# Kernel tuning notes

Measured on AMD Instinct MI355X. Metric: run time of the kernel, lower is better.

## Reference

```python
import jax, jax.numpy as jnp
import numpy as np

B, Q, K, H, V = 16, 128, 512, 256, 256


def setup_inputs() -> dict:
    key = jax.random.key(0)
    ks = jax.random.split(key, 7)
    return {
        "queries": jax.random.normal(ks[0], (B, Q, H), dtype=jnp.float32),
        "keys": jax.random.normal(ks[1], (B, K, H), dtype=jnp.float32),
        "values": jax.random.normal(ks[2], (B, K, V), dtype=jnp.float32),
        "Wq": jax.random.normal(ks[3], (H, H), dtype=jnp.float32) / np.sqrt(H),
        "Wk": jax.random.normal(ks[4], (H, H), dtype=jnp.float32) / np.sqrt(H),
        "Wv": jax.random.normal(ks[5], (H,), dtype=jnp.float32) / np.sqrt(H),
        "valid_lens": jax.random.randint(ks[6], (B,), 1, K + 1, dtype=jnp.int32),
    }


def reference(queries, keys, values, Wq, Wk, Wv, valid_lens):
    # Projections (no bias, matching nn.Linear(..., bias=False))
    q = jnp.einsum("bqd,hd->bqh", queries, Wq)  # W_q: weight is [out,in] in torch; symmetric here
    k = jnp.einsum("bkd,hd->bkh", keys, Wk)
    # Broadcast add -> tanh -> project to scalar score: [B, Q, K]
    features = jnp.tanh(q[:, :, None, :] + k[:, None, :, :])  # [B,Q,K,H]
    scores = jnp.einsum("bqkh,h->bqk", features, Wv)
    # masked_softmax: positions >= valid_len get -1e6 before softmax
    mask = jnp.arange(K)[None, None, :] < valid_lens[:, None, None]  # [B,1,K]
    scores = jnp.where(mask, scores, -1e6)
    attn = jax.nn.softmax(scores, axis=-1)
    # dropout in eval mode = identity
    return jnp.einsum("bqk,bkv->bqv", attn, values)
```

## Files before the change

kernel.cpp:

```cpp
#include <hip/hip_runtime.h>

#define BQ   16
#define QLEN 128
#define KLEN 512
#define HD   256
#define VD   256

typedef __bf16 bf16x8 __attribute__((ext_vector_type(8)));
typedef __bf16 bf16x4 __attribute__((ext_vector_type(4)));
typedef float  f32x4  __attribute__((ext_vector_type(4)));

static __device__ __forceinline__ float fexp2(float x) {
#if __has_builtin(__builtin_amdgcn_exp2f)
    return __builtin_amdgcn_exp2f(x);
#else
    return exp2f(x);
#endif
}
static __device__ __forceinline__ float frcp(float x) {
#if __has_builtin(__builtin_amdgcn_rcpf)
    return __builtin_amdgcn_rcpf(x);
#else
    return 1.0f / x;
#endif
}

#define EXP_SCALE 2.8853900817779268f

__global__ __launch_bounds__(256) void conv_w(
    const float* __restrict__ Wq, const float* __restrict__ Wk,
    __bf16* __restrict__ hi, __bf16* __restrict__ lo)
{
    const int t = blockIdx.x * 256 + threadIdx.x;
    const int e = t * 4;
    const float* src = (e < 65536) ? (Wq + e) : (Wk + (e - 65536));
    float4 v = *(const float4*)src;
    float f[4] = {v.x, v.y, v.z, v.w};
    bf16x4 h, l;
    #pragma unroll
    for (int j = 0; j < 4; ++j) {
        __bf16 hv = (__bf16)f[j];
        h[j] = hv;
        l[j] = (__bf16)(f[j] - (float)hv);
    }
    *(bf16x4*)(hi + e) = h;
    *(bf16x4*)(lo + e) = l;
}

__global__ __launch_bounds__(256) void mfma_proj(
    const float* __restrict__ queries, const float* __restrict__ keys,
    const __bf16* __restrict__ Whi_g, const __bf16* __restrict__ Wlo_g,
    float* __restrict__ Eq, float* __restrict__ Ekt)
{
    __shared__ __bf16 Ahi_s[64][40];
    __shared__ __bf16 Alo_s[64][40];
    __shared__ __bf16 Whi_s[128][40];
    __shared__ __bf16 Wlo_s[128][40];

    const int t    = threadIdx.x;
    const int ln   = t & 63;
    const int w    = t >> 6;
    const int p    = ln & 15;
    const int quad = ln >> 4;
    const int bx = blockIdx.x, by = blockIdx.y;
    const bool isq = by < 32;
    const int row0 = by * 64;
    const int col0 = bx * 128;

    const float* Ag = isq ? (queries + (size_t)row0 * HD)
                          : (keys + (size_t)(row0 - 2048) * HD);
    const __bf16* Wh = Whi_g + (isq ? 0 : 65536);
    const __bf16* Wl = Wlo_g + (isq ? 0 : 65536);

    const int ar = t >> 2, ac = (t & 3) * 8;
    const int wr = t >> 1, wc = (t & 1) * 16;

    float4 pa0, pa1;
    uint4 ph0, ph1, pl0, pl1;
    {
        const float* ap = Ag + ar * HD + ac;
        pa0 = *(const float4*)ap;
        pa1 = *(const float4*)(ap + 4);
        const size_t wb = (size_t)(col0 + wr) * HD + wc;
        ph0 = *(const uint4*)(Wh + wb);
        ph1 = *(const uint4*)(Wh + wb + 8);
        pl0 = *(const uint4*)(Wl + wb);
        pl1 = *(const uint4*)(Wl + wb + 8);
    }

    f32x4 acc[4][2] = {};

    for (int s = 0; s < 8; ++s) {
        __syncthreads();
        {
            float f[8] = {pa0.x, pa0.y, pa0.z, pa0.w, pa1.x, pa1.y, pa1.z, pa1.w};
            bf16x8 h, l;
            #pragma unroll
            for (int j = 0; j < 8; ++j) {
                __bf16 hv = (__bf16)f[j];
                h[j] = hv;
                l[j] = (__bf16)(f[j] - (float)hv);
            }
            *(bf16x8*)&Ahi_s[ar][ac] = h;
            *(bf16x8*)&Alo_s[ar][ac] = l;
            *(uint4*)&Whi_s[wr][wc]     = ph0;
            *(uint4*)&Whi_s[wr][wc + 8] = ph1;
            *(uint4*)&Wlo_s[wr][wc]     = pl0;
            *(uint4*)&Wlo_s[wr][wc + 8] = pl1;
        }
        __syncthreads();
        if (s < 7) {
            const int kc = (s + 1) * 32;
            const float* ap = Ag + ar * HD + kc + ac;
            pa0 = *(const float4*)ap;
            pa1 = *(const float4*)(ap + 4);
            const size_t wb = (size_t)(col0 + wr) * HD + kc + wc;
            ph0 = *(const uint4*)(Wh + wb);
            ph1 = *(const uint4*)(Wh + wb + 8);
            pl0 = *(const uint4*)(Wl + wb);
            pl1 = *(const uint4*)(Wl + wb + 8);
        }
        bf16x8 ah[4], al[4], bh[2], bl[2];
        #pragma unroll
        for (int mi = 0; mi < 4; ++mi) {
            ah[mi] = *(const bf16x8*)&Ahi_s[mi * 16 + p][quad * 8];
            al[mi] = *(const bf16x8*)&Alo_s[mi * 16 + p][quad * 8];
        }
        #pragma unroll
        for (int ci = 0; ci < 2; ++ci) {
            const int hrow = w * 32 + ci * 16 + p;
            bh[ci] = *(const bf16x8*)&Whi_s[hrow][quad * 8];
            bl[ci] = *(const bf16x8*)&Wlo_s[hrow][quad * 8];
        }
        #pragma unroll
        for (int mi = 0; mi < 4; ++mi)
            #pragma unroll
            for (int ci = 0; ci < 2; ++ci) {
                acc[mi][ci] = __builtin_amdgcn_mfma_f32_16x16x32_bf16(ah[mi], bh[ci], acc[mi][ci], 0, 0, 0);
                acc[mi][ci] = __builtin_amdgcn_mfma_f32_16x16x32_bf16(ah[mi], bl[ci], acc[mi][ci], 0, 0, 0);
                acc[mi][ci] = __builtin_amdgcn_mfma_f32_16x16x32_bf16(al[mi], bh[ci], acc[mi][ci], 0, 0, 0);
            }
    }

    #pragma unroll
    for (int mi = 0; mi < 4; ++mi)
        #pragma unroll
        for (int ci = 0; ci < 2; ++ci) {
            const int H  = col0 + w * 32 + ci * 16 + p;
            const int rl = mi * 16 + quad * 4;
            float e0 = fexp2(acc[mi][ci][0] * EXP_SCALE);
            float e1 = fexp2(acc[mi][ci][1] * EXP_SCALE);
            float e2 = fexp2(acc[mi][ci][2] * EXP_SCALE);
            float e3 = fexp2(acc[mi][ci][3] * EXP_SCALE);
            if (isq) {
                float* dst = Eq + (size_t)(row0 + rl) * HD + H;
                dst[0] = e0; dst[HD] = e1; dst[2 * HD] = e2; dst[3 * HD] = e3;
            } else {
                const int kr = row0 - 2048 + rl;
                const int b = kr >> 9, k0 = kr & 511;
                float4 st; st.x = e0; st.y = e1; st.z = e2; st.w = e3;
                *(float4*)(Ekt + ((size_t)b * HD + H) * KLEN + k0) = st;
            }
        }
}

__global__ __launch_bounds__(256) void proj_exp_gemm(
    const float* __restrict__ Qin, const float* __restrict__ Kin,
    const float* __restrict__ Wq, const float* __restrict__ Wk,
    float* __restrict__ Eq, float* __restrict__ Ekt)
{
    __shared__ union {
        struct { float a[2][16][68]; float w[2][16][68]; } s;
        float tb[64][65];
    } sh;

    const int t  = threadIdx.x;
    const int tx = t & 15, ty = t >> 4;
    const int bx = blockIdx.x, by = blockIdx.y;
    const bool isq = by < 32;
    const int row0 = isq ? by * 64 : (by - 32) * 64;
    const float* A = isq ? Qin : Kin;
    const float* W = isq ? Wq : Wk;
    const int lrow = t >> 2, ld0 = (t & 3) * 4;
    const float* Ab = A + (row0 + lrow) * HD;
    const float* Wb = W + (bx * 64 + lrow) * HD;

    float4 av = *(const float4*)(Ab + ld0);
    float4 wv = *(const float4*)(Wb + ld0);
    sh.s.a[0][ld0 + 0][lrow] = av.x; sh.s.a[0][ld0 + 1][lrow] = av.y;
    sh.s.a[0][ld0 + 2][lrow] = av.z; sh.s.a[0][ld0 + 3][lrow] = av.w;
    sh.s.w[0][ld0 + 0][lrow] = wv.x; sh.s.w[0][ld0 + 1][lrow] = wv.y;
    sh.s.w[0][ld0 + 2][lrow] = wv.z; sh.s.w[0][ld0 + 3][lrow] = wv.w;

    float acc[4][4] = {};
    int p = 0;
    for (int kc = 0; kc < HD; kc += 16) {
        if (kc + 16 < HD) {
            av = *(const float4*)(Ab + kc + 16 + ld0);
            wv = *(const float4*)(Wb + kc + 16 + ld0);
        }
        __syncthreads();
        if (kc + 16 < HD) {
            const int np = p ^ 1;
            sh.s.a[np][ld0 + 0][lrow] = av.x; sh.s.a[np][ld0 + 1][lrow] = av.y;
            sh.s.a[np][ld0 + 2][lrow] = av.z; sh.s.a[np][ld0 + 3][lrow] = av.w;
            sh.s.w[np][ld0 + 0][lrow] = wv.x; sh.s.w[np][ld0 + 1][lrow] = wv.y;
            sh.s.w[np][ld0 + 2][lrow] = wv.z; sh.s.w[np][ld0 + 3][lrow] = wv.w;
        }
        #pragma unroll
        for (int dd = 0; dd < 16; ++dd) {
            float4 a4 = *(const float4*)&sh.s.a[p][dd][ty * 4];
            float4 w4 = *(const float4*)&sh.s.w[p][dd][tx * 4];
            const float* af = (const float*)&a4;
            const float* wf = (const float*)&w4;
            #pragma unroll
            for (int i = 0; i < 4; ++i)
                #pragma unroll
                for (int j = 0; j < 4; ++j)
                    acc[i][j] = fmaf(af[i], wf[j], acc[i][j]);
        }
        p ^= 1;
    }

    float e[4][4];
    #pragma unroll
    for (int i = 0; i < 4; ++i)
        #pragma unroll
        for (int j = 0; j < 4; ++j)
            e[i][j] = fexp2(acc[i][j] * EXP_SCALE);

    if (isq) {
        float* Cb = Eq + (row0 + ty * 4) * HD + bx * 64 + tx * 4;
        #pragma unroll
        for (int i = 0; i < 4; ++i) {
            float4 st; st.x = e[i][0]; st.y = e[i][1]; st.z = e[i][2]; st.w = e[i][3];
            *(float4*)(Cb + i * HD) = st;
        }
    } else {
        __syncthreads();
        #pragma unroll
        for (int j = 0; j < 4; ++j) {
            float4 st; st.x = e[0][j]; st.y = e[1][j]; st.z = e[2][j]; st.w = e[3][j];
            *(float4*)&sh.tb[tx * 4 + j][ty * 4] = st;
        }
        __syncthreads();
        const int r = t >> 2, c0 = (t & 3) * 16;
        const int b = row0 >> 9, kbase = row0 & 511;
        float* dst = Ekt + ((size_t)b * HD + bx * 64 + r) * KLEN + kbase + c0;
        #pragma unroll
        for (int u = 0; u < 4; ++u) {
            float4 v = *(const float4*)&sh.tb[r][c0 + u * 4];
            *(float4*)(dst + u * 4) = v;
        }
    }
}

__global__ __launch_bounds__(512, 4) void fused_attn(
    const float* __restrict__ Eq, const float* __restrict__ Ekt,
    const float* __restrict__ values, const float* __restrict__ Wv,
    const int* __restrict__ vlen, float* __restrict__ out)
{
    __shared__ float eq_s[4][HD];
    __shared__ float wv_s[HD];
    __shared__ float sc[4][KLEN];
    __shared__ float ps[4][4][KLEN];
    __shared__ float wred[4];

    const int t    = threadIdx.x;
    const int b    = blockIdx.x >> 5;
    const int q0   = (blockIdx.x & 31) * 4;
    const int lane = t & 63;
    const int wid  = t >> 6;

    {
        const int h = t & 255, rr = t >> 8;
        eq_s[rr][h]     = Eq[(b * QLEN + q0 + rr) * HD + h];
        eq_s[rr + 2][h] = Eq[(b * QLEN + q0 + rr + 2) * HD + h];
        if (t < HD) {
            float w = Wv[t];
            wv_s[t] = w;
            float ws = w;
            #pragma unroll
            for (int off = 32; off > 0; off >>= 1) ws += __shfl_xor(ws, off, 64);
            if (lane == 0) wred[wid] = ws;
        }
    }
    __syncthreads();
    const float wv_sum = wred[0] + wred[1] + wred[2] + wred[3];

    const int hs    = wid & 3, khalf = wid >> 2;
    const int hbase = hs * 64;
    const int k4    = khalf * 256 + lane * 4;
    const float* ek = Ekt + ((size_t)b * HD + hbase) * KLEN + k4;
    float acc[4][4] = {};
    for (int hh = 0; hh < 64; hh += 4) {
        float4 e0 = *(const float4*)(ek + (size_t)(hh + 0) * KLEN);
        float4 e1 = *(const float4*)(ek + (size_t)(hh + 1) * KLEN);
        float4 e2 = *(const float4*)(ek + (size_t)(hh + 2) * KLEN);
        float4 e3 = *(const float4*)(ek + (size_t)(hh + 3) * KLEN);
        const float* E0 = (const float*)&e0;
        const float* E1 = (const float*)&e1;
        const float* E2 = (const float*)&e2;
        const float* E3 = (const float*)&e3;
        const float w0 = wv_s[hbase + hh + 0], w1 = wv_s[hbase + hh + 1];
        const float w2 = wv_s[hbase + hh + 2], w3 = wv_s[hbase + hh + 3];
        #pragma unroll
        for (int i = 0; i < 4; ++i) {
            const float a0 = eq_s[i][hbase + hh + 0], a1 = eq_s[i][hbase + hh + 1];
            const float a2 = eq_s[i][hbase + hh + 2], a3 = eq_s[i][hbase + hh + 3];
            #pragma unroll
            for (int j = 0; j < 4; ++j) {
                float d0 = fmaf(a0, E0[j], 1.f);
                float d1 = fmaf(a1, E1[j], 1.f);
                float d2 = fmaf(a2, E2[j], 1.f);
                float d3 = fmaf(a3, E3[j], 1.f);
                float d01 = d0 * d1, d23 = d2 * d3;
                float n01 = fmaf(w1, d0, w0 * d1);
                float n23 = fmaf(w3, d2, w2 * d3);
                float top = fmaf(n23, d01, n01 * d23);
                acc[i][j] = fmaf(top, frcp(d01 * d23), acc[i][j]);
            }
        }
    }
    #pragma unroll
    for (int i = 0; i < 4; ++i) {
        float4 st; st.x = acc[i][0]; st.y = acc[i][1]; st.z = acc[i][2]; st.w = acc[i][3];
        *(float4*)&ps[hs][i][k4] = st;
    }
    __syncthreads();

    {
        const int q = t >> 7, kk = (t & 127) * 4;
        float4 s0 = *(const float4*)&ps[0][q][kk];
        float4 s1 = *(const float4*)&ps[1][q][kk];
        float4 s2 = *(const float4*)&ps[2][q][kk];
        float4 s3 = *(const float4*)&ps[3][q][kk];
        float4 r;
        r.x = fmaf(-2.f, s0.x + s1.x + s2.x + s3.x, wv_sum);
        r.y = fmaf(-2.f, s0.y + s1.y + s2.y + s3.y, wv_sum);
        r.z = fmaf(-2.f, s0.z + s1.z + s2.z + s3.z, wv_sum);
        r.w = fmaf(-2.f, s0.w + s1.w + s2.w + s3.w, wv_sum);
        *(float4*)&sc[q][kk] = r;
    }
    __syncthreads();

    if (wid < 4) {
        const int len = vlen[b];
        float s[8];
        float m = -3.0e38f;
        #pragma unroll
        for (int j = 0; j < 8; ++j) {
            int k = lane + j * 64;
            float v = sc[wid][k];
            v = (k < len) ? v : -1.0e6f;
            s[j] = v;
            m = fmaxf(m, v);
        }
        #pragma unroll
        for (int off = 32; off > 0; off >>= 1) m = fmaxf(m, __shfl_xor(m, off, 64));
        float sum = 0.f;
        #pragma unroll
        for (int j = 0; j < 8; ++j) {
            float ev = fexp2(1.4426950408889634f * (s[j] - m));
            s[j] = ev;
            sum += ev;
        }
        #pragma unroll
        for (int off = 32; off > 0; off >>= 1) sum += __shfl_xor(sum, off, 64);
        const float rs = frcp(sum);
        #pragma unroll
        for (int j = 0; j < 8; ++j) sc[wid][lane + j * 64] = s[j] * rs;
    }
    __syncthreads();

    float (*po)[4][VD] = (float (*)[4][VD])ps;
    const int c4 = lane * 4;
    const float* vb = values + (size_t)b * KLEN * VD + (size_t)(wid * 64) * VD + c4;
    float o[4][4] = {};
    for (int kk = 0; kk < 64; kk += 4) {
        const int k = wid * 64 + kk;
        float4 pr[4];
        pr[0] = *(const float4*)&sc[0][k];
        pr[1] = *(const float4*)&sc[1][k];
        pr[2] = *(const float4*)&sc[2][k];
        pr[3] = *(const float4*)&sc[3][k];
        #pragma unroll
        for (int j = 0; j < 4; ++j) {
            float4 v4 = *(const float4*)(vb + (size_t)(kk + j) * VD);
            #pragma unroll
            for (int r = 0; r < 4; ++r) {
                float pj = ((const float*)&pr[r])[j];
                o[r][0] = fmaf(pj, v4.x, o[r][0]);
                o[r][1] = fmaf(pj, v4.y, o[r][1]);
                o[r][2] = fmaf(pj, v4.z, o[r][2]);
                o[r][3] = fmaf(pj, v4.w, o[r][3]);
            }
        }
    }
    #pragma unroll
    for (int r = 0; r < 4; ++r) {
        float4 st; st.x = o[r][0]; st.y = o[r][1]; st.z = o[r][2]; st.w = o[r][3];
        *(float4*)&po[wid][r][c4] = st;
    }
    __syncthreads();

    #pragma unroll
    for (int u = 0; u < 2; ++u) {
        int idx = t + u * 512;
        int r = idx >> 8, c = idx & 255;
        float s = 0.f;
        #pragma unroll
        for (int sl = 0; sl < 8; ++sl) s += po[sl][r][c];
        out[(b * QLEN + q0 + r) * VD + c] = s;
    }
}

extern "C" void kernel_launch(void* const* d_in, const int* in_sizes, int n_in,
                              void* d_out, int out_size, void* d_ws, size_t ws_size,
                              hipStream_t stream) {
    const float* queries = (const float*)d_in[0];
    const float* keys    = (const float*)d_in[1];
    const float* values  = (const float*)d_in[2];
    const float* Wq      = (const float*)d_in[3];
    const float* Wk      = (const float*)d_in[4];
    const float* Wv      = (const float*)d_in[5];
    const int*   vl      = (const int*)d_in[6];
    float* out = (float*)d_out;

    float* Eq  = (float*)d_ws;
    float* Ekt = Eq + 2048 * 256;

    if (ws_size >= 11010048) {
        __bf16* Whi = (__bf16*)(Ekt + 16 * HD * KLEN);
        __bf16* Wlo = Whi + 131072;
        conv_w<<<dim3(128), 256, 0, stream>>>(Wq, Wk, Whi, Wlo);
        mfma_proj<<<dim3(2, 160), 256, 0, stream>>>(queries, keys, Whi, Wlo, Eq, Ekt);
    } else {
        proj_exp_gemm<<<dim3(4, 160), 256, 0, stream>>>(queries, keys, Wq, Wk, Eq, Ekt);
    }
    fused_attn<<<dim3(512), 512, 0, stream>>>(Eq, Ekt, values, Wv, vl, out);
}
```

Baseline: 123.9 us.

## Fuse weight split into projection and skip masked key work by valid length

Removes the separate weight-conversion kernel and instead splits the fp32 weights into bf16 hi/lo parts inside the projection kernel. Key projection tiles lying wholly beyond the valid length return early, and the attention kernel skips score and value accumulation for key ranges past valid_len, zero-filling partial sums. The block-index mapping is reordered so batches interleave across blocks, which spreads the uneven per-batch work more evenly. Masked keys get a softmax weight of exactly zero, so skipping them is legitimate. The cost is redundant weight conversion in every block and some extra branching.

```diff
diff --git a/kernel.cpp b/kernel.cpp
--- a/kernel.cpp
+++ b/kernel.cpp
@@ -27,29 +27,10 @@
 
 #define EXP_SCALE 2.8853900817779268f
 
-__global__ __launch_bounds__(256) void conv_w(
-    const float* __restrict__ Wq, const float* __restrict__ Wk,
-    __bf16* __restrict__ hi, __bf16* __restrict__ lo)
-{
-    const int t = blockIdx.x * 256 + threadIdx.x;
-    const int e = t * 4;
-    const float* src = (e < 65536) ? (Wq + e) : (Wk + (e - 65536));
-    float4 v = *(const float4*)src;
-    float f[4] = {v.x, v.y, v.z, v.w};
-    bf16x4 h, l;
-    #pragma unroll
-    for (int j = 0; j < 4; ++j) {
-        __bf16 hv = (__bf16)f[j];
-        h[j] = hv;
-        l[j] = (__bf16)(f[j] - (float)hv);
-    }
-    *(bf16x4*)(hi + e) = h;
-    *(bf16x4*)(lo + e) = l;
-}
-
 __global__ __launch_bounds__(256) void mfma_proj(
     const float* __restrict__ queries, const float* __restrict__ keys,
-    const __bf16* __restrict__ Whi_g, const __bf16* __restrict__ Wlo_g,
+    const float* __restrict__ Wq, const float* __restrict__ Wk,
+    const int* __restrict__ vlen,
     float* __restrict__ Eq, float* __restrict__ Ekt)
 {
     __shared__ __bf16 Ahi_s[64][40];
@@ -67,25 +48,26 @@
     const int row0 = by * 64;
     const int col0 = bx * 128;
 
+    if (!isq) {
+        const int kr0 = row0 - 2048;
+        if ((kr0 & 511) >= vlen[kr0 >> 9]) return;
+    }
+
     const float* Ag = isq ? (queries + (size_t)row0 * HD)
                           : (keys + (size_t)(row0 - 2048) * HD);
-    const __bf16* Wh = Whi_g + (isq ? 0 : 65536);
-    const __bf16* Wl = Wlo_g + (isq ? 0 : 65536);
+    const float* Wg = isq ? Wq : Wk;
 
     const int ar = t >> 2, ac = (t & 3) * 8;
     const int wr = t >> 1, wc = (t & 1) * 16;
 
-    float4 pa0, pa1;
-    uint4 ph0, ph1, pl0, pl1;
+    float4 pa0, pa1, pw0, pw1, pw2, pw3;
     {
         const float* ap = Ag + ar * HD + ac;
         pa0 = *(const float4*)ap;
         pa1 = *(const float4*)(ap + 4);
-        const size_t wb = (size_t)(col0 + wr) * HD + wc;
-        ph0 = *(const uint4*)(Wh + wb);
-        ph1 = *(const uint4*)(Wh + wb + 8);
-        pl0 = *(const uint4*)(Wl + wb);
-        pl1 = *(const uint4*)(Wl + wb + 8);
+        const float* wp = Wg + (size_t)(col0 + wr) * HD + wc;
+        pw0 = *(const float4*)wp;       pw1 = *(const float4*)(wp + 4);
+        pw2 = *(const float4*)(wp + 8); pw3 = *(const float4*)(wp + 12);
     }
 
     f32x4 acc[4][2] = {};
@@ -93,20 +75,33 @@
     for (int s = 0; s < 8; ++s) {
         __syncthreads();
         {
-            float f[8] = {pa0.x, pa0.y, pa0.z, pa0.w, pa1.x, pa1.y, pa1.z, pa1.w};
+            float fa[8] = {pa0.x, pa0.y, pa0.z, pa0.w, pa1.x, pa1.y, pa1.z, pa1.w};
             bf16x8 h, l;
             #pragma unroll
             for (int j = 0; j < 8; ++j) {
-                __bf16 hv = (__bf16)f[j];
+                __bf16 hv = (__bf16)fa[j];
                 h[j] = hv;
-                l[j] = (__bf16)(f[j] - (float)hv);
+                l[j] = (__bf16)(fa[j] - (float)hv);
             }
             *(bf16x8*)&Ahi_s[ar][ac] = h;
             *(bf16x8*)&Alo_s[ar][ac] = l;
-            *(uint4*)&Whi_s[wr][wc]     = ph0;
-            *(uint4*)&Whi_s[wr][wc + 8] = ph1;
-            *(uint4*)&Wlo_s[wr][wc]     = pl0;
-            *(uint4*)&Wlo_s[wr][wc + 8] = pl1;
+
+            float fw[16] = {pw0.x, pw0.y, pw0.z, pw0.w, pw1.x, pw1.y, pw1.z, pw1.w,
+                            pw2.x, pw2.y, pw2.z, pw2.w, pw3.x, pw3.y, pw3.z, pw3.w};
+            bf16x8 wh0, wh1, wl0, wl1;
+            #pragma unroll
+            for (int j = 0; j < 8; ++j) {
+                __bf16 hv = (__bf16)fw[j];
+                wh0[j] = hv;
+                wl0[j] = (__bf16)(fw[j] - (float)hv);
+                __bf16 hv1 = (__bf16)fw[8 + j];
+                wh1[j] = hv1;
+                wl1[j] = (__bf16)(fw[8 + j] - (float)hv1);
+            }
+            *(bf16x8*)&Whi_s[wr][wc]     = wh0;
+            *(bf16x8*)&Whi_s[wr][wc + 8] = wh1;
+            *(bf16x8*)&Wlo_s[wr][wc]     = wl0;
+            *(bf16x8*)&Wlo_s[wr][wc + 8] = wl1;
         }
         __syncthreads();
         if (s < 7) {
@@ -114,11 +109,9 @@
             const float* ap = Ag + ar * HD + kc + ac;
             pa0 = *(const float4*)ap;
             pa1 = *(const float4*)(ap + 4);
-            const size_t wb = (size_t)(col0 + wr) * HD + kc + wc;
-            ph0 = *(const uint4*)(Wh + wb);
-            ph1 = *(const uint4*)(Wh + wb + 8);
-            pl0 = *(const uint4*)(Wl + wb);
-            pl1 = *(const uint4*)(Wl + wb + 8);
+            const float* wp = Wg + (size_t)(col0 + wr) * HD + kc + wc;
+            pw0 = *(const float4*)wp;       pw1 = *(const float4*)(wp + 4);
+            pw2 = *(const float4*)(wp + 8); pw3 = *(const float4*)(wp + 12);
         }
         bf16x8 ah[4], al[4], bh[2], bl[2];
         #pragma unroll
@@ -267,10 +260,11 @@
     __shared__ float wred[4];
 
     const int t    = threadIdx.x;
-    const int b    = blockIdx.x >> 5;
-    const int q0   = (blockIdx.x & 31) * 4;
+    const int b    = blockIdx.x & 15;
+    const int q0   = (blockIdx.x >> 4) * 4;
     const int lane = t & 63;
     const int wid  = t >> 6;
+    const int len  = vlen[b];
 
     {
         const int h = t & 255, rr = t >> 8;
@@ -289,43 +283,45 @@
     const float wv_sum = wred[0] + wred[1] + wred[2] + wred[3];
 
     const int hs    = wid & 3, khalf = wid >> 2;
-    const int hbase = hs * 64;
-    const int k4    = khalf * 256 + lane * 4;
-    const float* ek = Ekt + ((size_t)b * HD + hbase) * KLEN + k4;
-    float acc[4][4] = {};
-    for (int hh = 0; hh < 64; hh += 4) {
-        float4 e0 = *(const float4*)(ek + (size_t)(hh + 0) * KLEN);
-        float4 e1 = *(const float4*)(ek + (size_t)(hh + 1) * KLEN);
-        float4 e2 = *(const float4*)(ek + (size_t)(hh + 2) * KLEN);
-        float4 e3 = *(const float4*)(ek + (size_t)(hh + 3) * KLEN);
-        const float* E0 = (const float*)&e0;
-        const float* E1 = (const float*)&e1;
-        const float* E2 = (const float*)&e2;
-        const float* E3 = (const float*)&e3;
-        const float w0 = wv_s[hbase + hh + 0], w1 = wv_s[hbase + hh + 1];
-        const float w2 = wv_s[hbase + hh + 2], w3 = wv_s[hbase + hh + 3];
+    if (khalf * 256 < len) {
+        const int hbase = hs * 64;
+        const int k4    = khalf * 256 + lane * 4;
+        const float* ek = Ekt + ((size_t)b * HD + hbase) * KLEN + k4;
+        float acc[4][4] = {};
+        for (int hh = 0; hh < 64; hh += 4) {
+            float4 e0 = *(const float4*)(ek + (size_t)(hh + 0) * KLEN);
+            float4 e1 = *(const float4*)(ek + (size_t)(hh + 1) * KLEN);
+            float4 e2 = *(const float4*)(ek + (size_t)(hh + 2) * KLEN);
+            float4 e3 = *(const float4*)(ek + (size_t)(hh + 3) * KLEN);
+            const float* E0 = (const float*)&e0;
+            const float* E1 = (const float*)&e1;
+            const float* E2 = (const float*)&e2;
+            const float* E3 = (const float*)&e3;
+            const float w0 = wv_s[hbase + hh + 0], w1 = wv_s[hbase + hh + 1];
+            const float w2 = wv_s[hbase + hh + 2], w3 = wv_s[hbase + hh + 3];
+            #pragma unroll
+            for (int i = 0; i < 4; ++i) {
+                const float a0 = eq_s[i][hbase + hh + 0], a1 = eq_s[i][hbase + hh + 1];
+                const float a2 = eq_s[i][hbase + hh + 2], a3 = eq_s[i][hbase + hh + 3];
+                #pragma unroll
+                for (int j = 0; j < 4; ++j) {
+                    float d0 = fmaf(a0, E0[j], 1.f);
+                    float d1 = fmaf(a1, E1[j], 1.f);
+                    float d2 = fmaf(a2, E2[j], 1.f);
+                    float d3 = fmaf(a3, E3[j], 1.f);
+                    float d01 = d0 * d1, d23 = d2 * d3;
+                    float n01 = fmaf(w1, d0, w0 * d1);
+                    float n23 = fmaf(w3, d2, w2 * d3);
+                    float top = fmaf(n23, d01, n01 * d23);
+                    acc[i][j] = fmaf(top, frcp(d01 * d23), acc[i][j]);
+                }
+            }
+        }
         #pragma unroll
         for (int i = 0; i < 4; ++i) {
-            const float a0 = eq_s[i][hbase + hh + 0], a1 = eq_s[i][hbase + hh + 1];
-            const float a2 = eq_s[i][hbase + hh + 2], a3 = eq_s[i][hbase + hh + 3];
-            #pragma unroll
-            for (int j = 0; j < 4; ++j) {
-                float d0 = fmaf(a0, E0[j], 1.f);
-                float d1 = fmaf(a1, E1[j], 1.f);
-                float d2 = fmaf(a2, E2[j], 1.f);
-                float d3 = fmaf(a3, E3[j], 1.f);
-                float d01 = d0 * d1, d23 = d2 * d3;
-                float n01 = fmaf(w1, d0, w0 * d1);
-                float n23 = fmaf(w3, d2, w2 * d3);
-                float top = fmaf(n23, d01, n01 * d23);
-                acc[i][j] = fmaf(top, frcp(d01 * d23), acc[i][j]);
-            }
-        }
-    }
-    #pragma unroll
-    for (int i = 0; i < 4; ++i) {
-        float4 st; st.x = acc[i][0]; st.y = acc[i][1]; st.z = acc[i][2]; st.w = acc[i][3];
-        *(float4*)&ps[hs][i][k4] = st;
+            float4 st; st.x = acc[i][0]; st.y = acc[i][1]; st.z = acc[i][2]; st.w = acc[i][3];
+            *(float4*)&ps[hs][i][k4] = st;
+        }
     }
     __syncthreads();
 
@@ -345,7 +341,6 @@
     __syncthreads();
 
     if (wid < 4) {
-        const int len = vlen[b];
         float s[8];
         float m = -3.0e38f;
         #pragma unroll
@@ -375,32 +370,38 @@
 
     float (*po)[4][VD] = (float (*)[4][VD])ps;
     const int c4 = lane * 4;
-    const float* vb = values + (size_t)b * KLEN * VD + (size_t)(wid * 64) * VD + c4;
-    float o[4][4] = {};
-    for (int kk = 0; kk < 64; kk += 4) {
-        const int k = wid * 64 + kk;
-        float4 pr[4];
-        pr[0] = *(const float4*)&sc[0][k];
-        pr[1] = *(const float4*)&sc[1][k];
-        pr[2] = *(const float4*)&sc[2][k];
-        pr[3] = *(const float4*)&sc[3][k];
-        #pragma unroll
-        for (int j = 0; j < 4; ++j) {
-            float4 v4 = *(const float4*)(vb + (size_t)(kk + j) * VD);
-            #pragma unroll
-            for (int r = 0; r < 4; ++r) {
-                float pj = ((const float*)&pr[r])[j];
-                o[r][0] = fmaf(pj, v4.x, o[r][0]);
-                o[r][1] = fmaf(pj, v4.y, o[r][1]);
-                o[r][2] = fmaf(pj, v4.z, o[r][2]);
-                o[r][3] = fmaf(pj, v4.w, o[r][3]);
-            }
-        }
-    }
-    #pragma unroll
-    for (int r = 0; r < 4; ++r) {
-        float4 st; st.x = o[r][0]; st.y = o[r][1]; st.z = o[r][2]; st.w = o[r][3];
-        *(float4*)&po[wid][r][c4] = st;
+    if (wid * 64 < len) {
+        const float* vb = values + (size_t)b * KLEN * VD + (size_t)(wid * 64) * VD + c4;
+        float o[4][4] = {};
+        for (int kk = 0; kk < 64; kk += 4) {
+            const int k = wid * 64 + kk;
+            float4 pr[4];
+            pr[0] = *(const float4*)&sc[0][k];
+            pr[1] = *(const float4*)&sc[1][k];
+            pr[2] = *(const float4*)&sc[2][k];
+            pr[3] = *(const float4*)&sc[3][k];
+            #pragma unroll
+            for (int j = 0; j < 4; ++j) {
+                float4 v4 = *(const float4*)(vb + (size_t)(kk + j) * VD);
+                #pragma unroll
+                for (int r = 0; r < 4; ++r) {
+                    float pj = ((const float*)&pr[r])[j];
+                    o[r][0] = fmaf(pj, v4.x, o[r][0]);
+                    o[r][1] = fmaf(pj, v4.y, o[r][1]);
+                    o[r][2] = fmaf(pj, v4.z, o[r][2]);
+                    o[r][3] = fmaf(pj, v4.w, o[r][3]);
+                }
+            }
+        }
+        #pragma unroll
+        for (int r = 0; r < 4; ++r) {
+            float4 st; st.x = o[r][0]; st.y = o[r][1]; st.z = o[r][2]; st.w = o[r][3];
+            *(float4*)&po[wid][r][c4] = st;
+        }
+    } else {
+        float4 z; z.x = z.y = z.z = z.w = 0.f;
+        #pragma unroll
+        for (int r = 0; r < 4; ++r) *(float4*)&po[wid][r][c4] = z;
     }
     __syncthreads();
 
@@ -430,11 +431,8 @@
     float* Eq  = (float*)d_ws;
     float* Ekt = Eq + 2048 * 256;
 
-    if (ws_size >= 11010048) {
-        __bf16* Whi = (__bf16*)(Ekt + 16 * HD * KLEN);
-        __bf16* Wlo = Whi + 131072;
-        conv_w<<<dim3(128), 256, 0, stream>>>(Wq, Wk, Whi, Wlo);
-        mfma_proj<<<dim3(2, 160), 256, 0, stream>>>(queries, keys, Whi, Wlo, Eq, Ekt);
+    if (ws_size >= 10485760) {
+        mfma_proj<<<dim3(2, 160), 256, 0, stream>>>(queries, keys, Wq, Wk, vl, Eq, Ekt);
     } else {
         proj_exp_gemm<<<dim3(4, 160), 256, 0, stream>>>(queries, keys, Wq, Wk, Eq, Ekt);
     }
```

Result: faster. 121.0 us (-2.3%).
